# Performance work log

Hardware: AMD Instinct MI355X
Metric: run time of the kernel (lower is better)

Reference implementation:

```python
import jax, jax.numpy as jnp
import numpy as np

DIM_CAP = 16   # capsule dim
NCLS = 17      # annotation_nr
BS = 16
T = 120        # chunk_size * fps
P = 22         # players per frame graph
G = BS * T     # number of graphs = 1920
N = G * P      # nodes = 42240
C_IN = 14
CHS = [16, 32, 64, 152]  # 8m,16m,32m,76m with m=2
BN_EPS = 1e-3


def _build_graph():
    # fully-connected directed edges within each 22-node graph (no self loops)
    ii, jj = np.meshgrid(np.arange(P), np.arange(P), indexing='ij')
    mask = ii != jj
    li, lj = ii[mask], jj[mask]               # (462,)
    base = (np.arange(G) * P)[:, None]
    src = (base + li[None, :]).reshape(-1)
    dst = (base + lj[None, :]).reshape(-1)
    edge_index = np.stack([src, dst]).astype(np.int64)   # (2, E)
    batch = np.repeat(np.arange(G), P).astype(np.int64)  # (N,)
    return jnp.asarray(edge_index), jnp.asarray(batch)


def setup_inputs() -> dict:
    key = jax.random.key(0)
    ks = jax.random.split(key, 16)
    edge_index, batch = _build_graph()
    E = edge_index.shape[1]
    x = jax.random.normal(ks[0], (N, C_IN), dtype=jnp.float32)
    edge_attr = jax.random.uniform(ks[1], (E, 5), dtype=jnp.float32)
    dims = [C_IN] + CHS
    params = {}
    for i in range(4):
        s = 1.0 / np.sqrt(dims[i])
        params[f'W{i+1}'] = jax.random.normal(ks[2 + i], (dims[i], dims[i + 1]), dtype=jnp.float32) * s
        params[f'b{i+1}'] = jnp.zeros((dims[i + 1],), dtype=jnp.float32)
    c_out = DIM_CAP * NCLS  # 272
    params['conv_w'] = jax.random.normal(ks[6], (c_out, CHS[-1], 3), dtype=jnp.float32) * (1.0 / np.sqrt(CHS[-1] * 3))
    params['conv_b'] = jnp.zeros((c_out,), dtype=jnp.float32)
    params['bn_gamma'] = jnp.ones((T,), dtype=jnp.float32)
    params['bn_beta'] = jnp.zeros((T,), dtype=jnp.float32)
    return dict(x=x, edge_index=edge_index, batch=batch, edge_attr=edge_attr, **params)


def _gcn_layer(x, src, dst, w_edge, W, b):
    # PyG GCNConv: x' = D^-1/2 (A + I) D^-1/2 (x W) + b, edge weights w, self-loop weight 1
    n = x.shape[0]
    h = x @ W
    loop = jnp.arange(n)
    src_f = jnp.concatenate([src, loop])
    dst_f = jnp.concatenate([dst, loop])
    w_f = jnp.concatenate([w_edge, jnp.ones((n,), h.dtype)])
    deg = jax.ops.segment_sum(w_f, dst_f, num_segments=n)
    dinv = jnp.where(deg > 0, jax.lax.rsqrt(deg), 0.0)
    norm = dinv[src_f] * w_f * dinv[dst_f]
    out = jax.ops.segment_sum(norm[:, None] * h[src_f], dst_f, num_segments=n)
    return out + b


def reference(x, edge_index, batch, edge_attr, W1, b1, W2, b2, W3, b3, W4, b4,
              conv_w, conv_b, bn_gamma, bn_beta):
    src, dst = edge_index[0], edge_index[1]
    ew = edge_attr[:, 4]
    h = jax.nn.relu(_gcn_layer(x, src, dst, ew, W1, b1))
    h = jax.nn.relu(_gcn_layer(h, src, dst, ew, W2, b2))
    h = jax.nn.relu(_gcn_layer(h, src, dst, ew, W3, b3))
    h = jax.nn.relu(_gcn_layer(h, src, dst, ew, W4, b4))
    # global mean pool per graph -> (G, 152)
    ones = jnp.ones((h.shape[0],), h.dtype)
    cnt = jax.ops.segment_sum(ones, batch, num_segments=G)
    pooled = jax.ops.segment_sum(h, batch, num_segments=G) / jnp.clip(cnt, 1.0)[:, None]
    # (BS, T, 152) -> (BS, 152, T); conv kernel (3,1) with pad (1,1) on T
    feat = pooled.reshape(BS, T, CHS[-1]).transpose(0, 2, 1)
    conv = jax.lax.conv_general_dilated(
        feat, conv_w, window_strides=(1,), padding=[(1, 1)],
        dimension_numbers=('NCH', 'OIH', 'NCH'))
    conv = conv + conv_b[None, :, None]            # (BS, 272, T)
    caps = conv.transpose(0, 2, 1).reshape(BS, T, DIM_CAP, NCLS)
    # BatchNorm2d(num_features=T) in eval mode: running mean 0, var 1
    scale = (bn_gamma / jnp.sqrt(1.0 + BN_EPS))[None, :, None, None]
    shift = bn_beta[None, :, None, None]
    s = jax.nn.sigmoid(caps * scale + shift)
    out = jnp.sqrt(jnp.sum(jnp.square(s - 0.5), axis=2) * 4.0 / DIM_CAP)
    return out  # (BS, T, NCLS)
```

## Files before the change

### kernel.cpp

```cpp
#include <hip/hip_runtime.h>
#include <hip/hip_bf16.h>

#define GROUPS 1920
#define CH4 152
#define BUFS 100

template<int DIN, int KR>
__device__ __forceinline__ void layerA(const float* buf, float* Ut,
                                       const float* A4, int tid)
{
    constexpr int NKT = DIN / KR;
    constexpr int NT = NKT * 12;
    if (tid < NT) {
        const int kt = tid / 12, pt = tid - kt * 12;
        const int g = pt / 3, ps = (pt - g * 3) * 8;
        const int col0 = g * 24 + ps;
        const int xcol = g * 24;
        float acc[KR][8];
        #pragma unroll
        for (int j = 0; j < KR; ++j)
            #pragma unroll
            for (int a = 0; a < 8; ++a) acc[j][a] = 0.f;
        #pragma unroll 2
        for (int q = 0; q < 22; ++q) {
            const float4 a0 = *(const float4*)(A4 + (q * 4 + g) * 28 + ps);
            const float4 a1 = *(const float4*)(A4 + (q * 4 + g) * 28 + ps + 4);
            float xv[KR];
            #pragma unroll
            for (int j = 0; j < KR; ++j) xv[j] = buf[(kt * KR + j) * BUFS + xcol + q];
            #pragma unroll
            for (int j = 0; j < KR; ++j) {
                acc[j][0] = fmaf(xv[j], a0.x, acc[j][0]);
                acc[j][1] = fmaf(xv[j], a0.y, acc[j][1]);
                acc[j][2] = fmaf(xv[j], a0.z, acc[j][2]);
                acc[j][3] = fmaf(xv[j], a0.w, acc[j][3]);
                acc[j][4] = fmaf(xv[j], a1.x, acc[j][4]);
                acc[j][5] = fmaf(xv[j], a1.y, acc[j][5]);
                acc[j][6] = fmaf(xv[j], a1.z, acc[j][6]);
                acc[j][7] = fmaf(xv[j], a1.w, acc[j][7]);
            }
        }
        #pragma unroll
        for (int j = 0; j < KR; ++j) {
            *(float4*)(Ut + (kt * KR + j) * BUFS + col0) =
                make_float4(acc[j][0], acc[j][1], acc[j][2], acc[j][3]);
            *(float4*)(Ut + (kt * KR + j) * BUFS + col0 + 4) =
                make_float4(acc[j][4], acc[j][5], acc[j][6], acc[j][7]);
        }
    }
}

template<int DIN, int DOUT, int CR>
__device__ __forceinline__ void layerB(const float* __restrict__ W,
                                       const float* __restrict__ B,
                                       const float* Ut, float* buf, int tid)
{
    constexpr int NCT = DOUT / CR;
    constexpr int NT = NCT * 12;
    if (tid < NT) {
        const int ct = tid / 12, pt = tid - ct * 12;
        const int p0 = pt * 8, c0 = ct * CR;
        float acc[CR][8];
        #pragma unroll
        for (int b = 0; b < CR; ++b) {
            const float bias = B[c0 + b];
            #pragma unroll
            for (int a = 0; a < 8; ++a) acc[b][a] = bias;
        }
        #pragma unroll 4
        for (int k = 0; k < DIN; ++k) {
            const float4 u0 = *(const float4*)(Ut + k * BUFS + p0);
            const float4 u1 = *(const float4*)(Ut + k * BUFS + p0 + 4);
            float wv[CR];
            #pragma unroll
            for (int b = 0; b < CR; b += 4) {
                const float4 w4 = *(const float4*)(W + k * DOUT + c0 + b);
                wv[b] = w4.x; wv[b + 1] = w4.y; wv[b + 2] = w4.z; wv[b + 3] = w4.w;
            }
            #pragma unroll
            for (int b = 0; b < CR; ++b) {
                acc[b][0] = fmaf(wv[b], u0.x, acc[b][0]);
                acc[b][1] = fmaf(wv[b], u0.y, acc[b][1]);
                acc[b][2] = fmaf(wv[b], u0.z, acc[b][2]);
                acc[b][3] = fmaf(wv[b], u0.w, acc[b][3]);
                acc[b][4] = fmaf(wv[b], u1.x, acc[b][4]);
                acc[b][5] = fmaf(wv[b], u1.y, acc[b][5]);
                acc[b][6] = fmaf(wv[b], u1.z, acc[b][6]);
                acc[b][7] = fmaf(wv[b], u1.w, acc[b][7]);
            }
        }
        #pragma unroll
        for (int b = 0; b < CR; ++b) {
            *(float4*)(buf + (c0 + b) * BUFS + p0) =
                make_float4(fmaxf(acc[b][0], 0.f), fmaxf(acc[b][1], 0.f),
                            fmaxf(acc[b][2], 0.f), fmaxf(acc[b][3], 0.f));
            *(float4*)(buf + (c0 + b) * BUFS + p0 + 4) =
                make_float4(fmaxf(acc[b][4], 0.f), fmaxf(acc[b][5], 0.f),
                            fmaxf(acc[b][6], 0.f), fmaxf(acc[b][7], 0.f));
        }
    }
}

__global__ __launch_bounds__(256) void gcn_kernel(
    const float* __restrict__ x, const float* __restrict__ ea,
    const float* __restrict__ W1, const float* __restrict__ b1,
    const float* __restrict__ W2, const float* __restrict__ b2,
    const float* __restrict__ W3, const float* __restrict__ b3,
    const float* __restrict__ W4, const float* __restrict__ b4,
    float* __restrict__ pooledT)
{
    __shared__ __align__(16) float A4[24 * 4 * 28];
    __shared__ __align__(16) float dv[4 * 24];
    __shared__ __align__(16) float buf[64 * BUFS];
    __shared__ __align__(16) float Ut[64 * BUFS];

    const int tid = threadIdx.x;
    const int G0 = blockIdx.x * 4;

    for (int idx = tid; idx < 24 * 4 * 28; idx += 256) {
        const int q = idx / 112, r = idx - q * 112;
        const int g = r / 28, p = r - g * 28;
        float v = 0.f;
        if (q < 22 && p < 22) {
            if (q == p) v = 1.0f;
            else {
                const int e = q * 21 + p - (p > q);
                v = ea[((size_t)(G0 + g) * 462 + e) * 5 + 4];
            }
        }
        A4[idx] = v;
    }
    for (int idx = tid; idx < 14 * 96; idx += 256) {
        const int k = idx / 96, col = idx - k * 96;
        const int g = col / 24, p = col - g * 24;
        buf[k * BUFS + col] = (p < 22) ? x[((size_t)(G0 + g) * 22 + p) * 14 + k] : 0.f;
    }
    __syncthreads();

    if (tid < 96) {
        const int g = tid / 24, p = tid - g * 24;
        float s = 0.f;
        #pragma unroll
        for (int q = 0; q < 22; ++q) s += A4[(q * 4 + g) * 28 + p];
        dv[tid] = (s > 0.f) ? rsqrtf(s) : 0.f;
    }
    __syncthreads();
    for (int idx = tid; idx < 24 * 4 * 28; idx += 256) {
        const int q = idx / 112, r = idx - q * 112;
        const int g = r / 28, p = r - g * 28;
        if (p < 24) A4[idx] *= dv[g * 24 + q] * dv[g * 24 + p];
    }
    __syncthreads();

    layerA<14, 2>(buf, Ut, A4, tid);  __syncthreads();
    layerB<14, 16, 4>(W1, b1, Ut, buf, tid);  __syncthreads();
    layerA<16, 4>(buf, Ut, A4, tid);  __syncthreads();
    layerB<16, 32, 4>(W2, b2, Ut, buf, tid);  __syncthreads();
    layerA<32, 4>(buf, Ut, A4, tid);  __syncthreads();
    layerB<32, 64, 8>(W3, b3, Ut, buf, tid);  __syncthreads();
    layerA<64, 4>(buf, Ut, A4, tid);  __syncthreads();

    float* pscr = buf;
    if (tid < 19 * 12) {
        const int ct = tid / 12, pt = tid - ct * 12;
        const int p0 = pt * 8, c0 = ct * 8;
        float acc[8][8];
        #pragma unroll
        for (int b = 0; b < 8; ++b) {
            const float bias = b4[c0 + b];
            #pragma unroll
            for (int a = 0; a < 8; ++a) acc[b][a] = bias;
        }
        #pragma unroll 4
        for (int k = 0; k < 64; ++k) {
            const float4 u0 = *(const float4*)(Ut + k * BUFS + p0);
            const float4 u1 = *(const float4*)(Ut + k * BUFS + p0 + 4);
            float wv[8];
            #pragma unroll
            for (int b = 0; b < 8; b += 4) {
                const float4 w4 = *(const float4*)(W4 + k * 152 + c0 + b);
                wv[b] = w4.x; wv[b + 1] = w4.y; wv[b + 2] = w4.z; wv[b + 3] = w4.w;
            }
            #pragma unroll
            for (int b = 0; b < 8; ++b) {
                acc[b][0] = fmaf(wv[b], u0.x, acc[b][0]);
                acc[b][1] = fmaf(wv[b], u0.y, acc[b][1]);
                acc[b][2] = fmaf(wv[b], u0.z, acc[b][2]);
                acc[b][3] = fmaf(wv[b], u0.w, acc[b][3]);
                acc[b][4] = fmaf(wv[b], u1.x, acc[b][4]);
                acc[b][5] = fmaf(wv[b], u1.y, acc[b][5]);
                acc[b][6] = fmaf(wv[b], u1.z, acc[b][6]);
                acc[b][7] = fmaf(wv[b], u1.w, acc[b][7]);
            }
        }
        const int alim = ((pt % 3) == 2) ? 6 : 8;
        float ps8[8];
        #pragma unroll
        for (int b = 0; b < 8; ++b) {
            float s = 0.f;
            #pragma unroll
            for (int a = 0; a < 8; ++a)
                s += (a < alim) ? fmaxf(acc[b][a], 0.f) : 0.f;
            ps8[b] = s;
        }
        *(float4*)(pscr + pt * 152 + c0) = make_float4(ps8[0], ps8[1], ps8[2], ps8[3]);
        *(float4*)(pscr + pt * 152 + c0 + 4) = make_float4(ps8[4], ps8[5], ps8[6], ps8[7]);
    }
    __syncthreads();

    if (tid < 152) {
        const int c = tid;
        const int b = G0 / 120, t0 = G0 - b * 120;
        float4 v;
        #pragma unroll
        for (int g = 0; g < 4; ++g) {
            const float s = pscr[(g * 3 + 0) * 152 + c] + pscr[(g * 3 + 1) * 152 + c]
                          + pscr[(g * 3 + 2) * 152 + c];
            ((float*)&v)[g] = s * (1.0f / 22.0f);
        }
        *(float4*)(pooledT + ((size_t)(b * 152 + c) * 128) + 4 + t0) = v;
    }
}

__global__ __launch_bounds__(256) void repack_conv_w(const float* __restrict__ cw,
                                                     float* __restrict__ wT,
                                                     float* __restrict__ pT)
{
    const int idx = blockIdx.x * 256 + threadIdx.x;
    if (idx < 272 * 456) {
        const int o = idx / 456, r = idx - o * 456;
        wT[r * 272 + o] = cw[idx];
    } else {
        const int j = idx - 272 * 456;
        if (j < 16 * 152 * 8) {
            const int row = j >> 3, s = j & 7;
            const int slot = (s < 4) ? s : s + 120;
            pT[(size_t)row * 128 + slot] = 0.f;
        }
    }
}

__global__ __launch_bounds__(320) void conv_caps_kernel(
    const float* __restrict__ pT, const float* __restrict__ wT,
    const float* __restrict__ cb, const float* __restrict__ gamma,
    const float* __restrict__ beta, float* __restrict__ out)
{
    __shared__ __align__(16) float s2[8 * 272];
    __shared__ float sc[8], sh[8];

    const int bx = blockIdx.x;
    const int b = bx / 15, tile = bx - b * 15;
    const int t0 = tile * 8;
    const int tid = threadIdx.x;

    if (tid < 8) {
        const int t = t0 + tid;
        sc[tid] = gamma[t] * 0.999500374688f;
        sh[tid] = beta[t];
    }
    __syncthreads();

    if (tid < 272) {
        const int o = tid;
        const float cb0 = cb[o];
        float acc[8];
        #pragma unroll
        for (int tt = 0; tt < 8; ++tt) acc[tt] = cb0;
        const float* wp0 = wT + o;
        const float* frow0 = pT + ((size_t)b * 152) * 128 + 3 + t0;
        float w0 = wp0[0], w1 = wp0[272], w2 = wp0[544];
        #pragma unroll 2
        for (int i = 0; i < CH4; ++i) {
            const int inext = (i == CH4 - 1) ? i : i + 1;
            const float* nwp = wp0 + inext * 816;
            const float nw0 = nwp[0], nw1 = nwp[272], nw2 = nwp[544];
            const float* f = frow0 + (size_t)i * 128;
            float fr[10];
            #pragma unroll
            for (int j = 0; j < 10; ++j) fr[j] = f[j];
            #pragma unroll
            for (int tt = 0; tt < 8; ++tt)
                acc[tt] = fmaf(w0, fr[tt], fmaf(w1, fr[tt + 1], fmaf(w2, fr[tt + 2], acc[tt])));
            w0 = nw0; w1 = nw1; w2 = nw2;
        }
        #pragma unroll
        for (int tt = 0; tt < 8; ++tt) {
            const float z = fmaf(acc[tt], sc[tt], sh[tt]);
            const float s = 1.0f / (1.0f + __expf(-z));
            const float d = s - 0.5f;
            s2[tt * 272 + o] = d * d;
        }
    }
    __syncthreads();

    for (int e = tid; e < 8 * 17; e += 320) {
        const int tt = e / 17, n = e - tt * 17;
        float s = 0.f;
        #pragma unroll
        for (int d = 0; d < 16; ++d) s += s2[tt * 272 + d * 17 + n];
        out[((size_t)b * 120 + t0 + tt) * 17 + n] = sqrtf(s) * 0.5f;
    }
}

extern "C" void kernel_launch(void* const* d_in, const int* in_sizes, int n_in,
                              void* d_out, int out_size, void* d_ws, size_t ws_size,
                              hipStream_t stream) {
    const float* x     = (const float*)d_in[0];
    const float* ea    = (const float*)d_in[3];
    const float* W1    = (const float*)d_in[4];
    const float* b1    = (const float*)d_in[5];
    const float* W2    = (const float*)d_in[6];
    const float* b2    = (const float*)d_in[7];
    const float* W3    = (const float*)d_in[8];
    const float* b3    = (const float*)d_in[9];
    const float* W4    = (const float*)d_in[10];
    const float* b4    = (const float*)d_in[11];
    const float* cw    = (const float*)d_in[12];
    const float* cb    = (const float*)d_in[13];
    const float* gamma = (const float*)d_in[14];
    const float* beta  = (const float*)d_in[15];
    float* out = (float*)d_out;

    float* pT = (float*)d_ws;
    float* wT = pT + (size_t)16 * 152 * 128;

    hipLaunchKernelGGL(repack_conv_w, dim3((272 * 456 + 16 * 152 * 8 + 255) / 256),
                       dim3(256), 0, stream, cw, wT, pT);
    hipLaunchKernelGGL(gcn_kernel, dim3(GROUPS / 4), dim3(256), 0, stream,
                       x, ea, W1, b1, W2, b2, W3, b3, W4, b4, pT);
    hipLaunchKernelGGL(conv_caps_kernel, dim3(16 * 15), dim3(320), 0, stream,
                       pT, wT, cb, gamma, beta, out);
}
```

Measured before the change: 169.3 us.

## Process one graph per 64-thread block and halve conv time tile

The GCN kernel now handles a single 22-node graph per one-wavefront block instead of four graphs per 256-thread block. The shared-memory layout changes to node-major activations with vectorized K loads, and per-thread register tiles are reshaped. The conv kernel uses 4 time steps per block with 480 blocks instead of 8 with 240, and the padding offsets in the pooled buffer change to match. The aim is more blocks and higher occupancy across CUs with less idle-thread waste. The cost is more redundant weight loads and less per-block reuse.

```diff
diff --git a/kernel.cpp b/kernel.cpp
--- a/kernel.cpp
+++ b/kernel.cpp
@@ -3,105 +3,112 @@
 
 #define GROUPS 1920
 #define CH4 152
-#define BUFS 100
+#define BXS 68
+#define UTS 28
+#define AS  28
+
+template<int KR>
+__device__ __forceinline__ void loadK(const float* p, float* xk) {
+    if constexpr (KR == 2) {
+        float2 v = *(const float2*)p; xk[0] = v.x; xk[1] = v.y;
+    } else if constexpr (KR == 4) {
+        float4 v = *(const float4*)p;
+        xk[0] = v.x; xk[1] = v.y; xk[2] = v.z; xk[3] = v.w;
+    } else {
+        float4 v0 = *(const float4*)p, v1 = *(const float4*)(p + 4);
+        xk[0] = v0.x; xk[1] = v0.y; xk[2] = v0.z; xk[3] = v0.w;
+        xk[4] = v1.x; xk[5] = v1.y; xk[6] = v1.z; xk[7] = v1.w;
+    }
+}
 
 template<int DIN, int KR>
-__device__ __forceinline__ void layerA(const float* buf, float* Ut,
-                                       const float* A4, int tid)
+__device__ __forceinline__ void layerA(const float* bufX, float* Ut,
+                                       const float* A, int lane)
 {
     constexpr int NKT = DIN / KR;
-    constexpr int NT = NKT * 12;
-    if (tid < NT) {
-        const int kt = tid / 12, pt = tid - kt * 12;
-        const int g = pt / 3, ps = (pt - g * 3) * 8;
-        const int col0 = g * 24 + ps;
-        const int xcol = g * 24;
-        float acc[KR][8];
+    const int kt = lane / 6, pt = lane % 6;
+    if (kt < NKT) {
+        const int p0 = pt * 4, k0 = kt * KR;
+        float acc[KR][4];
         #pragma unroll
         for (int j = 0; j < KR; ++j)
             #pragma unroll
-            for (int a = 0; a < 8; ++a) acc[j][a] = 0.f;
+            for (int a = 0; a < 4; ++a) acc[j][a] = 0.f;
         #pragma unroll 2
         for (int q = 0; q < 22; ++q) {
-            const float4 a0 = *(const float4*)(A4 + (q * 4 + g) * 28 + ps);
-            const float4 a1 = *(const float4*)(A4 + (q * 4 + g) * 28 + ps + 4);
-            float xv[KR];
-            #pragma unroll
-            for (int j = 0; j < KR; ++j) xv[j] = buf[(kt * KR + j) * BUFS + xcol + q];
+            const float4 a4 = *(const float4*)(A + q * AS + p0);
+            float xk[KR];
+            loadK<KR>(bufX + q * BXS + k0, xk);
             #pragma unroll
             for (int j = 0; j < KR; ++j) {
-                acc[j][0] = fmaf(xv[j], a0.x, acc[j][0]);
-                acc[j][1] = fmaf(xv[j], a0.y, acc[j][1]);
-                acc[j][2] = fmaf(xv[j], a0.z, acc[j][2]);
-                acc[j][3] = fmaf(xv[j], a0.w, acc[j][3]);
-                acc[j][4] = fmaf(xv[j], a1.x, acc[j][4]);
-                acc[j][5] = fmaf(xv[j], a1.y, acc[j][5]);
-                acc[j][6] = fmaf(xv[j], a1.z, acc[j][6]);
-                acc[j][7] = fmaf(xv[j], a1.w, acc[j][7]);
-            }
-        }
-        #pragma unroll
-        for (int j = 0; j < KR; ++j) {
-            *(float4*)(Ut + (kt * KR + j) * BUFS + col0) =
+                acc[j][0] = fmaf(xk[j], a4.x, acc[j][0]);
+                acc[j][1] = fmaf(xk[j], a4.y, acc[j][1]);
+                acc[j][2] = fmaf(xk[j], a4.z, acc[j][2]);
+                acc[j][3] = fmaf(xk[j], a4.w, acc[j][3]);
+            }
+        }
+        #pragma unroll
+        for (int j = 0; j < KR; ++j)
+            *(float4*)(Ut + (k0 + j) * UTS + p0) =
                 make_float4(acc[j][0], acc[j][1], acc[j][2], acc[j][3]);
-            *(float4*)(Ut + (kt * KR + j) * BUFS + col0 + 4) =
-                make_float4(acc[j][4], acc[j][5], acc[j][6], acc[j][7]);
-        }
     }
 }
 
 template<int DIN, int DOUT, int CR>
 __device__ __forceinline__ void layerB(const float* __restrict__ W,
                                        const float* __restrict__ B,
-                                       const float* Ut, float* buf, int tid)
+                                       const float* Ut, float* bufX, int lane)
 {
     constexpr int NCT = DOUT / CR;
-    constexpr int NT = NCT * 12;
-    if (tid < NT) {
-        const int ct = tid / 12, pt = tid - ct * 12;
-        const int p0 = pt * 8, c0 = ct * CR;
-        float acc[CR][8];
+    const int ct = lane / 6, pt = lane % 6;
+    if (ct < NCT) {
+        const int p0 = pt * 4, c0 = ct * CR;
+        float acc[CR][4];
         #pragma unroll
         for (int b = 0; b < CR; ++b) {
             const float bias = B[c0 + b];
             #pragma unroll
-            for (int a = 0; a < 8; ++a) acc[b][a] = bias;
-        }
-        #pragma unroll 4
+            for (int a = 0; a < 4; ++a) acc[b][a] = bias;
+        }
+        #pragma unroll 2
         for (int k = 0; k < DIN; ++k) {
-            const float4 u0 = *(const float4*)(Ut + k * BUFS + p0);
-            const float4 u1 = *(const float4*)(Ut + k * BUFS + p0 + 4);
+            const float4 u4 = *(const float4*)(Ut + k * UTS + p0);
             float wv[CR];
-            #pragma unroll
-            for (int b = 0; b < CR; b += 4) {
-                const float4 w4 = *(const float4*)(W + k * DOUT + c0 + b);
-                wv[b] = w4.x; wv[b + 1] = w4.y; wv[b + 2] = w4.z; wv[b + 3] = w4.w;
+            if constexpr (CR == 2) {
+                float2 w2 = *(const float2*)(W + k * DOUT + c0);
+                wv[0] = w2.x; wv[1] = w2.y;
+            } else {
+                #pragma unroll
+                for (int b = 0; b < CR; b += 4) {
+                    float4 w4 = *(const float4*)(W + k * DOUT + c0 + b);
+                    wv[b] = w4.x; wv[b+1] = w4.y; wv[b+2] = w4.z; wv[b+3] = w4.w;
+                }
             }
             #pragma unroll
             for (int b = 0; b < CR; ++b) {
-                acc[b][0] = fmaf(wv[b], u0.x, acc[b][0]);
-                acc[b][1] = fmaf(wv[b], u0.y, acc[b][1]);
-                acc[b][2] = fmaf(wv[b], u0.z, acc[b][2]);
-                acc[b][3] = fmaf(wv[b], u0.w, acc[b][3]);
-                acc[b][4] = fmaf(wv[b], u1.x, acc[b][4]);
-                acc[b][5] = fmaf(wv[b], u1.y, acc[b][5]);
-                acc[b][6] = fmaf(wv[b], u1.z, acc[b][6]);
-                acc[b][7] = fmaf(wv[b], u1.w, acc[b][7]);
-            }
-        }
-        #pragma unroll
-        for (int b = 0; b < CR; ++b) {
-            *(float4*)(buf + (c0 + b) * BUFS + p0) =
-                make_float4(fmaxf(acc[b][0], 0.f), fmaxf(acc[b][1], 0.f),
-                            fmaxf(acc[b][2], 0.f), fmaxf(acc[b][3], 0.f));
-            *(float4*)(buf + (c0 + b) * BUFS + p0 + 4) =
-                make_float4(fmaxf(acc[b][4], 0.f), fmaxf(acc[b][5], 0.f),
-                            fmaxf(acc[b][6], 0.f), fmaxf(acc[b][7], 0.f));
-        }
-    }
-}
-
-__global__ __launch_bounds__(256) void gcn_kernel(
+                acc[b][0] = fmaf(wv[b], u4.x, acc[b][0]);
+                acc[b][1] = fmaf(wv[b], u4.y, acc[b][1]);
+                acc[b][2] = fmaf(wv[b], u4.z, acc[b][2]);
+                acc[b][3] = fmaf(wv[b], u4.w, acc[b][3]);
+            }
+        }
+        #pragma unroll
+        for (int a = 0; a < 4; ++a) {
+            float* dst = bufX + (p0 + a) * BXS + c0;
+            if constexpr (CR == 2) {
+                *(float2*)dst = make_float2(fmaxf(acc[0][a], 0.f), fmaxf(acc[1][a], 0.f));
+            } else {
+                #pragma unroll
+                for (int b = 0; b < CR; b += 4)
+                    *(float4*)(dst + b) =
+                        make_float4(fmaxf(acc[b][a], 0.f), fmaxf(acc[b+1][a], 0.f),
+                                    fmaxf(acc[b+2][a], 0.f), fmaxf(acc[b+3][a], 0.f));
+            }
+        }
+    }
+}
+
+__global__ __launch_bounds__(64) void gcn_kernel(
     const float* __restrict__ x, const float* __restrict__ ea,
     const float* __restrict__ W1, const float* __restrict__ b1,
     const float* __restrict__ W2, const float* __restrict__ b2,
@@ -109,116 +116,100 @@
     const float* __restrict__ W4, const float* __restrict__ b4,
     float* __restrict__ pooledT)
 {
-    __shared__ __align__(16) float A4[24 * 4 * 28];
-    __shared__ __align__(16) float dv[4 * 24];
-    __shared__ __align__(16) float buf[64 * BUFS];
-    __shared__ __align__(16) float Ut[64 * BUFS];
-
-    const int tid = threadIdx.x;
-    const int G0 = blockIdx.x * 4;
-
-    for (int idx = tid; idx < 24 * 4 * 28; idx += 256) {
-        const int q = idx / 112, r = idx - q * 112;
-        const int g = r / 28, p = r - g * 28;
+    __shared__ __align__(16) float A[24 * AS];
+    __shared__ __align__(16) float dv[24];
+    __shared__ __align__(16) float bufX[24 * BXS];
+    __shared__ __align__(16) float Ut[64 * UTS];
+
+    const int lane = threadIdx.x;
+    const int g = blockIdx.x;
+
+    for (int idx = lane; idx < 24 * AS; idx += 64) {
+        const int q = idx / AS, p = idx - q * AS;
         float v = 0.f;
-        if (q < 22 && p < 22) {
-            if (q == p) v = 1.0f;
-            else {
-                const int e = q * 21 + p - (p > q);
-                v = ea[((size_t)(G0 + g) * 462 + e) * 5 + 4];
-            }
-        }
-        A4[idx] = v;
-    }
-    for (int idx = tid; idx < 14 * 96; idx += 256) {
-        const int k = idx / 96, col = idx - k * 96;
-        const int g = col / 24, p = col - g * 24;
-        buf[k * BUFS + col] = (p < 22) ? x[((size_t)(G0 + g) * 22 + p) * 14 + k] : 0.f;
-    }
-    __syncthreads();
-
-    if (tid < 96) {
-        const int g = tid / 24, p = tid - g * 24;
+        if (q < 22 && p < 22)
+            v = (q == p) ? 1.0f : ea[((size_t)g * 462 + q * 21 + p - (p > q)) * 5 + 4];
+        A[idx] = v;
+    }
+    for (int idx = lane; idx < 22 * 14; idx += 64) {
+        const int p = idx / 14, k = idx - p * 14;
+        bufX[p * BXS + k] = x[(size_t)g * (22 * 14) + idx];
+    }
+    __syncthreads();
+
+    if (lane < 24) {
         float s = 0.f;
         #pragma unroll
-        for (int q = 0; q < 22; ++q) s += A4[(q * 4 + g) * 28 + p];
-        dv[tid] = (s > 0.f) ? rsqrtf(s) : 0.f;
-    }
-    __syncthreads();
-    for (int idx = tid; idx < 24 * 4 * 28; idx += 256) {
-        const int q = idx / 112, r = idx - q * 112;
-        const int g = r / 28, p = r - g * 28;
-        if (p < 24) A4[idx] *= dv[g * 24 + q] * dv[g * 24 + p];
-    }
-    __syncthreads();
-
-    layerA<14, 2>(buf, Ut, A4, tid);  __syncthreads();
-    layerB<14, 16, 4>(W1, b1, Ut, buf, tid);  __syncthreads();
-    layerA<16, 4>(buf, Ut, A4, tid);  __syncthreads();
-    layerB<16, 32, 4>(W2, b2, Ut, buf, tid);  __syncthreads();
-    layerA<32, 4>(buf, Ut, A4, tid);  __syncthreads();
-    layerB<32, 64, 8>(W3, b3, Ut, buf, tid);  __syncthreads();
-    layerA<64, 4>(buf, Ut, A4, tid);  __syncthreads();
-
-    float* pscr = buf;
-    if (tid < 19 * 12) {
-        const int ct = tid / 12, pt = tid - ct * 12;
-        const int p0 = pt * 8, c0 = ct * 8;
-        float acc[8][8];
-        #pragma unroll
-        for (int b = 0; b < 8; ++b) {
-            const float bias = b4[c0 + b];
-            #pragma unroll
-            for (int a = 0; a < 8; ++a) acc[b][a] = bias;
-        }
-        #pragma unroll 4
-        for (int k = 0; k < 64; ++k) {
-            const float4 u0 = *(const float4*)(Ut + k * BUFS + p0);
-            const float4 u1 = *(const float4*)(Ut + k * BUFS + p0 + 4);
-            float wv[8];
-            #pragma unroll
-            for (int b = 0; b < 8; b += 4) {
-                const float4 w4 = *(const float4*)(W4 + k * 152 + c0 + b);
-                wv[b] = w4.x; wv[b + 1] = w4.y; wv[b + 2] = w4.z; wv[b + 3] = w4.w;
-            }
+        for (int q = 0; q < 22; ++q) s += A[q * AS + lane];
+        dv[lane] = (s > 0.f) ? rsqrtf(s) : 0.f;
+    }
+    __syncthreads();
+    for (int idx = lane; idx < 24 * AS; idx += 64) {
+        const int q = idx / AS, p = idx - q * AS;
+        if (p < 24) A[idx] *= dv[q] * dv[p];
+    }
+    __syncthreads();
+
+    layerA<14, 2>(bufX, Ut, A, lane);            __syncthreads();
+    layerB<14, 16, 2>(W1, b1, Ut, bufX, lane);   __syncthreads();
+    layerA<16, 2>(bufX, Ut, A, lane);            __syncthreads();
+    layerB<16, 32, 4>(W2, b2, Ut, bufX, lane);   __syncthreads();
+    layerA<32, 4>(bufX, Ut, A, lane);            __syncthreads();
+    layerB<32, 64, 8>(W3, b3, Ut, bufX, lane);   __syncthreads();
+    layerA<64, 8>(bufX, Ut, A, lane);            __syncthreads();
+
+    float* pscr = A;
+    {
+        const int ct = lane / 3, pt = lane - (lane / 3) * 3;
+        if (lane < 57) {
+            const int p0 = pt * 8, c0 = ct * 8;
+            float acc[8][8];
             #pragma unroll
             for (int b = 0; b < 8; ++b) {
-                acc[b][0] = fmaf(wv[b], u0.x, acc[b][0]);
-                acc[b][1] = fmaf(wv[b], u0.y, acc[b][1]);
-                acc[b][2] = fmaf(wv[b], u0.z, acc[b][2]);
-                acc[b][3] = fmaf(wv[b], u0.w, acc[b][3]);
-                acc[b][4] = fmaf(wv[b], u1.x, acc[b][4]);
-                acc[b][5] = fmaf(wv[b], u1.y, acc[b][5]);
-                acc[b][6] = fmaf(wv[b], u1.z, acc[b][6]);
-                acc[b][7] = fmaf(wv[b], u1.w, acc[b][7]);
-            }
-        }
-        const int alim = ((pt % 3) == 2) ? 6 : 8;
-        float ps8[8];
-        #pragma unroll
-        for (int b = 0; b < 8; ++b) {
-            float s = 0.f;
-            #pragma unroll
-            for (int a = 0; a < 8; ++a)
-                s += (a < alim) ? fmaxf(acc[b][a], 0.f) : 0.f;
-            ps8[b] = s;
-        }
-        *(float4*)(pscr + pt * 152 + c0) = make_float4(ps8[0], ps8[1], ps8[2], ps8[3]);
-        *(float4*)(pscr + pt * 152 + c0 + 4) = make_float4(ps8[4], ps8[5], ps8[6], ps8[7]);
-    }
-    __syncthreads();
-
-    if (tid < 152) {
-        const int c = tid;
-        const int b = G0 / 120, t0 = G0 - b * 120;
-        float4 v;
-        #pragma unroll
-        for (int g = 0; g < 4; ++g) {
-            const float s = pscr[(g * 3 + 0) * 152 + c] + pscr[(g * 3 + 1) * 152 + c]
-                          + pscr[(g * 3 + 2) * 152 + c];
-            ((float*)&v)[g] = s * (1.0f / 22.0f);
-        }
-        *(float4*)(pooledT + ((size_t)(b * 152 + c) * 128) + 4 + t0) = v;
+                const float bias = b4[c0 + b];
+                #pragma unroll
+                for (int a = 0; a < 8; ++a) acc[b][a] = bias;
+            }
+            #pragma unroll 2
+            for (int k = 0; k < 64; ++k) {
+                const float4 u0 = *(const float4*)(Ut + k * UTS + p0);
+                const float4 u1 = *(const float4*)(Ut + k * UTS + p0 + 4);
+                const float4 wa = *(const float4*)(W4 + k * 152 + c0);
+                const float4 wb = *(const float4*)(W4 + k * 152 + c0 + 4);
+                const float wv[8] = { wa.x, wa.y, wa.z, wa.w, wb.x, wb.y, wb.z, wb.w };
+                #pragma unroll
+                for (int b = 0; b < 8; ++b) {
+                    acc[b][0] = fmaf(wv[b], u0.x, acc[b][0]);
+                    acc[b][1] = fmaf(wv[b], u0.y, acc[b][1]);
+                    acc[b][2] = fmaf(wv[b], u0.z, acc[b][2]);
+                    acc[b][3] = fmaf(wv[b], u0.w, acc[b][3]);
+                    acc[b][4] = fmaf(wv[b], u1.x, acc[b][4]);
+                    acc[b][5] = fmaf(wv[b], u1.y, acc[b][5]);
+                    acc[b][6] = fmaf(wv[b], u1.z, acc[b][6]);
+                    acc[b][7] = fmaf(wv[b], u1.w, acc[b][7]);
+                }
+            }
+            const int alim = (pt == 2) ? 6 : 8;
+            float ps[8];
+            #pragma unroll
+            for (int b = 0; b < 8; ++b) {
+                float s = 0.f;
+                #pragma unroll
+                for (int a = 0; a < 8; ++a)
+                    s += (a < alim) ? fmaxf(acc[b][a], 0.f) : 0.f;
+                ps[b] = s;
+            }
+            *(float4*)(pscr + pt * 156 + c0)     = make_float4(ps[0], ps[1], ps[2], ps[3]);
+            *(float4*)(pscr + pt * 156 + c0 + 4) = make_float4(ps[4], ps[5], ps[6], ps[7]);
+        }
+    }
+    __syncthreads();
+    {
+        const int b = g / 120, t = g - b * 120;
+        for (int c = lane; c < 152; c += 64) {
+            const float s = pscr[c] + pscr[156 + c] + pscr[312 + c];
+            pooledT[((size_t)(b * 152 + c)) * 128 + 1 + t] = s * (1.0f / 22.0f);
+        }
     }
 }
 
@@ -234,7 +225,7 @@
         const int j = idx - 272 * 456;
         if (j < 16 * 152 * 8) {
             const int row = j >> 3, s = j & 7;
-            const int slot = (s < 4) ? s : s + 120;
+            const int slot = (s == 0) ? 0 : 120 + s;
             pT[(size_t)row * 128 + slot] = 0.f;
         }
     }
@@ -245,15 +236,15 @@
     const float* __restrict__ cb, const float* __restrict__ gamma,
     const float* __restrict__ beta, float* __restrict__ out)
 {
-    __shared__ __align__(16) float s2[8 * 272];
-    __shared__ float sc[8], sh[8];
+    __shared__ __align__(16) float s2[4 * 272];
+    __shared__ float sc[4], sh[4];
 
     const int bx = blockIdx.x;
-    const int b = bx / 15, tile = bx - b * 15;
-    const int t0 = tile * 8;
+    const int b = bx / 30, tile = bx - b * 30;
+    const int t0 = tile * 4;
     const int tid = threadIdx.x;
 
-    if (tid < 8) {
+    if (tid < 4) {
         const int t = t0 + tid;
         sc[tid] = gamma[t] * 0.999500374688f;
         sh[tid] = beta[t];
@@ -263,28 +254,23 @@
     if (tid < 272) {
         const int o = tid;
         const float cb0 = cb[o];
-        float acc[8];
-        #pragma unroll
-        for (int tt = 0; tt < 8; ++tt) acc[tt] = cb0;
-        const float* wp0 = wT + o;
-        const float* frow0 = pT + ((size_t)b * 152) * 128 + 3 + t0;
-        float w0 = wp0[0], w1 = wp0[272], w2 = wp0[544];
-        #pragma unroll 2
+        float acc[4] = { cb0, cb0, cb0, cb0 };
+        const float* fb = pT + (size_t)b * 152 * 128 + t0;
+        const float* wp = wT + o;
+        #pragma unroll 4
         for (int i = 0; i < CH4; ++i) {
-            const int inext = (i == CH4 - 1) ? i : i + 1;
-            const float* nwp = wp0 + inext * 816;
-            const float nw0 = nwp[0], nw1 = nwp[272], nw2 = nwp[544];
-            const float* f = frow0 + (size_t)i * 128;
-            float fr[10];
-            #pragma unroll
-            for (int j = 0; j < 10; ++j) fr[j] = f[j];
-            #pragma unroll
-            for (int tt = 0; tt < 8; ++tt)
+            const float4 fA = *(const float4*)(fb + i * 128);
+            const float4 fB = *(const float4*)(fb + i * 128 + 4);
+            const float fr[6] = { fA.x, fA.y, fA.z, fA.w, fB.x, fB.y };
+            const float w0 = wp[(i * 3 + 0) * 272];
+            const float w1 = wp[(i * 3 + 1) * 272];
+            const float w2 = wp[(i * 3 + 2) * 272];
+            #pragma unroll
+            for (int tt = 0; tt < 4; ++tt)
                 acc[tt] = fmaf(w0, fr[tt], fmaf(w1, fr[tt + 1], fmaf(w2, fr[tt + 2], acc[tt])));
-            w0 = nw0; w1 = nw1; w2 = nw2;
-        }
-        #pragma unroll
-        for (int tt = 0; tt < 8; ++tt) {
+        }
+        #pragma unroll
+        for (int tt = 0; tt < 4; ++tt) {
             const float z = fmaf(acc[tt], sc[tt], sh[tt]);
             const float s = 1.0f / (1.0f + __expf(-z));
             const float d = s - 0.5f;
@@ -293,7 +279,7 @@
     }
     __syncthreads();
 
-    for (int e = tid; e < 8 * 17; e += 320) {
+    for (int e = tid; e < 4 * 17; e += 320) {
         const int tt = e / 17, n = e - tt * 17;
         float s = 0.f;
         #pragma unroll
@@ -326,8 +312,8 @@
 
     hipLaunchKernelGGL(repack_conv_w, dim3((272 * 456 + 16 * 152 * 8 + 255) / 256),
                        dim3(256), 0, stream, cw, wT, pT);
-    hipLaunchKernelGGL(gcn_kernel, dim3(GROUPS / 4), dim3(256), 0, stream,
+    hipLaunchKernelGGL(gcn_kernel, dim3(GROUPS), dim3(64), 0, stream,
                        x, ea, W1, b1, W2, b2, W3, b3, W4, b4, pT);
-    hipLaunchKernelGGL(conv_caps_kernel, dim3(16 * 15), dim3(320), 0, stream,
+    hipLaunchKernelGGL(conv_caps_kernel, dim3(16 * 30), dim3(320), 0, stream,
                        pT, wT, cb, gamma, beta, out);
 }
```

New measurement: 171.1 us. No clear change (+1.1%).
